# Kernel optimization log

Measured on AMD Instinct MI355X. Metric: run time of the kernel, lower is better.

The kernel has to match this reference:

```python
import jax, jax.numpy as jnp
import numpy as np

D_MODEL = 768
NUM_HEADS = 12
DIM_QKV = D_MODEL // NUM_HEADS  # 64
NEG_INF = -1000000000.0


def setup_inputs() -> dict:
    key = jax.random.key(0)
    ks = jax.random.split(key, 12)
    B, S = 2, 2048
    def lin(kw, kb):
        # torch nn.Linear default init: U(-1/sqrt(fan_in), 1/sqrt(fan_in))
        bound = 1.0 / np.sqrt(D_MODEL)
        W = jax.random.uniform(kw, (D_MODEL, D_MODEL), jnp.float32, -bound, bound)
        b = jax.random.uniform(kb, (D_MODEL,), jnp.float32, -bound, bound)
        return W, b
    Wq, bq = lin(ks[0], ks[1])
    Wk, bk = lin(ks[2], ks[3])
    Wv, bv = lin(ks[4], ks[5])
    Wo, bo = lin(ks[6], ks[7])
    Q = jax.random.normal(ks[8], (B, S, D_MODEL), jnp.float32)
    K = jax.random.normal(ks[9], (B, S, D_MODEL), jnp.float32)
    V = jax.random.normal(ks[10], (B, S, D_MODEL), jnp.float32)
    mask = jnp.tril(jnp.ones((S, S), dtype=bool))[None, None]  # [1,1,S,S] causal
    return {"Q": Q, "K": K, "V": V, "mask": mask,
            "Wq": Wq, "bq": bq, "Wk": Wk, "bk": bk,
            "Wv": Wv, "bv": bv, "Wo": Wo, "bo": bo}


def _split_heads(x):
    B, S, _ = x.shape
    return x.reshape(B, S, NUM_HEADS, DIM_QKV).transpose(0, 2, 1, 3)  # [B,H,S,d]


def reference(Q, K, V, mask, Wq, bq, Wk, bk, Wv, bv, Wo, bo):
    # torch Linear: y = x @ W.T + b
    q = _split_heads(Q @ Wq.T + bq)
    k = _split_heads(K @ Wk.T + bk)
    v = _split_heads(V @ Wv.T + bv)
    scale = jnp.sqrt(jnp.float32(DIM_QKV))
    scores = jnp.einsum('bhqd,bhkd->bhqk', q, k) / scale  # [B,H,S,S]
    scores = jnp.where(mask, scores, NEG_INF)
    probs = jax.nn.softmax(scores, axis=-1)  # dropout p=0 -> identity
    attn = jnp.einsum('bhqk,bhkd->bhqd', probs, v)
    B, H, S, d = attn.shape
    out = attn.transpose(0, 2, 1, 3).reshape(B, S, H * d) @ Wo.T + bo
    return out, scores
```

## Files before the change

### kernel.cpp

```cpp
#include <hip/hip_runtime.h>
#include <hip/hip_bf16.h>

typedef __attribute__((ext_vector_type(8))) short short8;
typedef __attribute__((ext_vector_type(4))) short short4v;
typedef __attribute__((ext_vector_type(4))) float f32x4;

#define S_LEN 2048
#define DM 768
#define NH 12
#define HD 64
#define NB 2
#define MROWS (NB*S_LEN)
#define NEGINF (-1.0e9f)
#define XEL 3145728
#define WEL 589824

__device__ __forceinline__ unsigned short f2bf(float x) {
    __hip_bfloat16 h = __float2bfloat16(x);
    return *reinterpret_cast<unsigned short*>(&h);
}

__device__ __forceinline__ void gl_lds16(const unsigned short* g, unsigned short* l) {
    __builtin_amdgcn_global_load_lds(
        (const __attribute__((address_space(1))) unsigned int*)g,
        (__attribute__((address_space(3))) unsigned int*)l, 16, 0, 0);
}

__global__ __launch_bounds__(256) void cvt_w_kernel(
    const float* w0, const float* w1, const float* w2, const float* w3,
    unsigned short* dst)
{
    int which = blockIdx.y;
    const float* src = (which == 0) ? w0 : (which == 1) ? w1 : (which == 2) ? w2 : w3;
    size_t idx = (size_t)blockIdx.x * 256 + threadIdx.x;
    const float* s = src + idx * 8;
    f32x4 v0 = *(const f32x4*)s;
    f32x4 v1 = *(const f32x4*)(s + 4);
    short8 o;
    o[0] = (short)f2bf(v0[0]); o[1] = (short)f2bf(v0[1]);
    o[2] = (short)f2bf(v0[2]); o[3] = (short)f2bf(v0[3]);
    o[4] = (short)f2bf(v1[0]); o[5] = (short)f2bf(v1[1]);
    o[6] = (short)f2bf(v1[2]); o[7] = (short)f2bf(v1[3]);
    *(short8*)&dst[(size_t)which * WEL + idx * 8] = o;
}

__global__ __launch_bounds__(256) void gemm_qkv_kernel(
    const float* Xq, const float* Xk, const float* Xv, const unsigned short* Wall,
    const float* b0, const float* b1, const float* b2, unsigned short* qh)
{
    int by = blockIdx.y;
    const float* A = (by == 0) ? Xq : (by == 1) ? Xk : Xv;
    const unsigned short* W = Wall + (size_t)by * WEL;
    const float* bias = (by == 0) ? b0 : (by == 1) ? b1 : b2;
    int bx = blockIdx.x;
    int im = (bx & 7) + 8 * (bx / 48);
    int jn = (bx >> 3) % 6;
    int i0 = im * 128, j0 = jn * 128;

    __shared__ unsigned short As[128 * 64];
    __shared__ unsigned short Ws[128 * 64];

    int t = threadIdx.x;
    int w = t >> 6, lane = t & 63, g = lane >> 4, fr = lane & 15;
    int wm = w >> 1, wn = w & 1;

    f32x4 acc[4][4];
    for (int i = 0; i < 4; ++i)
        for (int j = 0; j < 4; ++j)
            acc[i][j] = (f32x4){0.f, 0.f, 0.f, 0.f};

    int boff = t * 16;
    int arow = t >> 3;
    int acol = (t & 7) * 8;

    for (int k0 = 0; k0 < DM; k0 += 64) {
        __syncthreads();
        for (int r = 0; r < 4; ++r) {
            int b = r * 4096 + boff;
            int row = b >> 7, colb = b & 127;
            gl_lds16(&W[(size_t)(j0 + row) * DM + k0 + (colb >> 1)],
                     (unsigned short*)((char*)Ws + b));
        }
        for (int rr = 0; rr < 4; ++rr) {
            int row = rr * 32 + arow;
            const float* src = &A[(size_t)(i0 + row) * DM + k0 + acol];
            f32x4 v0 = *(const f32x4*)src;
            f32x4 v1 = *(const f32x4*)(src + 4);
            short8 o;
            o[0] = (short)f2bf(v0[0]); o[1] = (short)f2bf(v0[1]);
            o[2] = (short)f2bf(v0[2]); o[3] = (short)f2bf(v0[3]);
            o[4] = (short)f2bf(v1[0]); o[5] = (short)f2bf(v1[1]);
            o[6] = (short)f2bf(v1[2]); o[7] = (short)f2bf(v1[3]);
            *(short8*)&As[row * 64 + acol] = o;
        }
        __syncthreads();
        for (int kk = 0; kk < 2; ++kk) {
            short8 af[4], wf[4];
            for (int it = 0; it < 4; ++it)
                af[it] = *(const short8*)&As[(wm * 64 + it * 16 + fr) * 64 + kk * 32 + g * 8];
            for (int jt = 0; jt < 4; ++jt)
                wf[jt] = *(const short8*)&Ws[(wn * 64 + jt * 16 + fr) * 64 + kk * 32 + g * 8];
            for (int it = 0; it < 4; ++it)
                for (int jt = 0; jt < 4; ++jt)
                    acc[it][jt] = __builtin_amdgcn_mfma_f32_16x16x32_bf16(af[it], wf[jt], acc[it][jt], 0, 0, 0);
        }
    }

    float scl = (by == 0) ? 0.125f : 1.0f;
    if (by < 2) {
        unsigned short* outp = qh + (size_t)by * XEL;
        for (int jt = 0; jt < 4; ++jt) {
            int j = j0 + wn * 64 + jt * 16 + fr;
            float bv = bias[j];
            int h = j >> 6, dq = j & 63;
            for (int it = 0; it < 4; ++it)
                for (int r = 0; r < 4; ++r) {
                    int i = i0 + wm * 64 + it * 16 + g * 4 + r;
                    int bb = i >> 11, s = i & 2047;
                    outp[((size_t)((bb * NH + h) * S_LEN) + s) * HD + dq] = f2bf((acc[it][jt][r] + bv) * scl);
                }
        }
    } else {
        unsigned short* vtp = qh + (size_t)2 * XEL;
        for (int jt = 0; jt < 4; ++jt) {
            int j = j0 + wn * 64 + jt * 16 + fr;
            float bv = bias[j];
            int h = j >> 6, dq = j & 63;
            for (int it = 0; it < 4; ++it) {
                int ibase = i0 + wm * 64 + it * 16 + g * 4;
                int bb = ibase >> 11, s = ibase & 2047;
                short4v o;
                for (int r = 0; r < 4; ++r) o[r] = (short)f2bf(acc[it][jt][r] + bv);
                *(short4v*)&vtp[((size_t)(bb * NH + h) * HD + dq) * S_LEN + s] = o;
            }
        }
    }
}

__global__ __launch_bounds__(256) void gemm_o_kernel(
    const unsigned short* A, const unsigned short* W, const float* bias, float* f_out)
{
    int bx = blockIdx.x;
    int im = (bx & 7) + 8 * (bx / 96);
    int jn = (bx >> 3) % 12;
    int i0 = im * 64, j0 = jn * 64;

    __shared__ unsigned short As[64 * 64];
    __shared__ unsigned short Ws[64 * 64];

    int t = threadIdx.x;
    int w = t >> 6, lane = t & 63, g = lane >> 4, fr = lane & 15;
    int wm = w >> 1, wn = w & 1;

    f32x4 acc[2][2];
    for (int i = 0; i < 2; ++i)
        for (int j = 0; j < 2; ++j)
            acc[i][j] = (f32x4){0.f, 0.f, 0.f, 0.f};

    int boff = t * 16;

    for (int k0 = 0; k0 < DM; k0 += 64) {
        __syncthreads();
        for (int r = 0; r < 2; ++r) {
            int b = r * 4096 + boff;
            int row = b >> 7, colb = b & 127;
            gl_lds16(&A[(size_t)(i0 + row) * DM + k0 + (colb >> 1)],
                     (unsigned short*)((char*)As + b));
            gl_lds16(&W[(size_t)(j0 + row) * DM + k0 + (colb >> 1)],
                     (unsigned short*)((char*)Ws + b));
        }
        __syncthreads();
        for (int kk = 0; kk < 2; ++kk) {
            short8 af[2], wf[2];
            for (int it = 0; it < 2; ++it)
                af[it] = *(const short8*)&As[(wm * 32 + it * 16 + fr) * 64 + kk * 32 + g * 8];
            for (int jt = 0; jt < 2; ++jt)
                wf[jt] = *(const short8*)&Ws[(wn * 32 + jt * 16 + fr) * 64 + kk * 32 + g * 8];
            for (int it = 0; it < 2; ++it)
                for (int jt = 0; jt < 2; ++jt)
                    acc[it][jt] = __builtin_amdgcn_mfma_f32_16x16x32_bf16(af[it], wf[jt], acc[it][jt], 0, 0, 0);
        }
    }

    for (int jt = 0; jt < 2; ++jt) {
        int j = j0 + wn * 32 + jt * 16 + fr;
        float bv = bias[j];
        for (int it = 0; it < 2; ++it)
            for (int r = 0; r < 4; ++r) {
                int i = i0 + wm * 32 + it * 16 + g * 4 + r;
                f_out[(size_t)i * DM + j] = acc[it][jt][r] + bv;
            }
    }
}

__global__ __launch_bounds__(256) void attn_kernel(
    const unsigned short* q, const unsigned short* k, const unsigned short* vt,
    float* scores, unsigned short* attn)
{
    __shared__ unsigned short KV[2][8192];
    __shared__ float P[4][16][68];
    int t = threadIdx.x;
    int w = t >> 6, lane = t & 63, g = lane >> 4, fr = lane & 15;
    float (*Pw)[68] = P[w];

    int bid = blockIdx.x;
    int bh = (bid & 7) * 3 + (bid >> 3) % 3;
    int s = bid / 24;
    int myspan = (w < 2) ? s : 63 - s;
    int qbase = myspan * 32 + (w & 1) * 16;
    int myNt = ((myspan * 32 + 31) >> 6) + 1;
    int ntmax = (((63 - s) * 32 + 31) >> 6) + 1;
    int b = bh / NH, h = bh % NH;

    const unsigned short* qp = q + (size_t)bh * S_LEN * HD;
    const unsigned short* kp = k + (size_t)bh * S_LEN * HD;
    const unsigned short* vp = vt + (size_t)bh * HD * S_LEN;
    float* sp = scores + (size_t)bh * S_LEN * S_LEN;

    int srow2 = t >> 3;
    int scb = (t & 7) * 16;
    int swzu = (fr & 7) * 8;

    short8 qf0 = *(const short8*)&qp[(size_t)(qbase + fr) * HD + g * 8];
    short8 qf1 = *(const short8*)&qp[(size_t)(qbase + fr) * HD + 32 + g * 8];

    f32x4 acc[4];
    for (int jt = 0; jt < 4; ++jt) acc[jt] = (f32x4){0.f, 0.f, 0.f, 0.f};
    float m_run = -1e30f, l_run = 0.f;

    for (int rd = 0; rd < 2; ++rd) {
        int row = rd * 32 + srow2;
        int sc = (scb ^ ((row & 7) << 4)) >> 1;
        gl_lds16(&kp[(size_t)row * HD + sc], &KV[0][(size_t)t * 8 + rd * 2048]);
        gl_lds16(&vp[(size_t)row * S_LEN + sc], &KV[0][4096 + (size_t)t * 8 + rd * 2048]);
    }
    __builtin_amdgcn_sched_barrier(0);
    asm volatile("s_waitcnt vmcnt(0)" ::: "memory");
    __builtin_amdgcn_sched_barrier(0);
    __builtin_amdgcn_s_barrier();
    __builtin_amdgcn_sched_barrier(0);

    int buf = 0;
    for (int kt = 0; kt < ntmax; ++kt) {
        if (kt + 1 < ntmax) {
            int kb2 = (kt + 1) * 64;
            for (int rd = 0; rd < 2; ++rd) {
                int row = rd * 32 + srow2;
                int sc = (scb ^ ((row & 7) << 4)) >> 1;
                gl_lds16(&kp[(size_t)(kb2 + row) * HD + sc], &KV[buf ^ 1][(size_t)t * 8 + rd * 2048]);
                gl_lds16(&vp[(size_t)row * S_LEN + kb2 + sc], &KV[buf ^ 1][4096 + (size_t)t * 8 + rd * 2048]);
            }
        }
        __builtin_amdgcn_sched_barrier(0);
        if (kt < myNt) {
            const unsigned short* Kb = KV[buf];
            const unsigned short* Vb = KV[buf] + 4096;
            int kb = kt * 64;
            bool diag = (kt == myNt - 1);

            short8 kf[4][2];
            for (int ktt = 0; ktt < 4; ++ktt) {
                int base = (ktt * 16 + fr) * 64;
                kf[ktt][0] = *(const short8*)&Kb[base + ((g * 8) ^ swzu)];
                kf[ktt][1] = *(const short8*)&Kb[base + ((32 + g * 8) ^ swzu)];
            }
            __builtin_amdgcn_s_setprio(1);
            f32x4 s4v[4];
            for (int ktt = 0; ktt < 4; ++ktt) {
                f32x4 s4 = (f32x4){0.f, 0.f, 0.f, 0.f};
                s4 = __builtin_amdgcn_mfma_f32_16x16x32_bf16(qf0, kf[ktt][0], s4, 0, 0, 0);
                s4 = __builtin_amdgcn_mfma_f32_16x16x32_bf16(qf1, kf[ktt][1], s4, 0, 0, 0);
                s4v[ktt] = s4;
            }
            __builtin_amdgcn_s_setprio(0);
            if (diag) {
                for (int ktt = 0; ktt < 4; ++ktt) {
                    int kg = kb + ktt * 16 + fr;
                    for (int r = 0; r < 4; ++r) {
                        int qg = qbase + g * 4 + r;
                        float val = (kg <= qg) ? s4v[ktt][r] : NEGINF;
                        Pw[g * 4 + r][ktt * 16 + fr] = val;
                    }
                }
            } else {
                for (int ktt = 0; ktt < 4; ++ktt)
                    for (int r = 0; r < 4; ++r)
                        Pw[g * 4 + r][ktt * 16 + fr] = s4v[ktt][r];
            }
            for (int pass = 0; pass < 4; ++pass) {
                int rr = pass * 4 + g;
                int cc = fr * 4;
                f32x4 vv = *(const f32x4*)&Pw[rr][cc];
                __builtin_nontemporal_store(vv, (f32x4*)&sp[(size_t)(qbase + rr) * S_LEN + kb + cc]);
            }
            f32x4 pA = *(const f32x4*)&Pw[fr][g * 8];
            f32x4 pB = *(const f32x4*)&Pw[fr][g * 8 + 4];
            f32x4 pC = *(const f32x4*)&Pw[fr][32 + g * 8];
            f32x4 pD = *(const f32x4*)&Pw[fr][32 + g * 8 + 4];
            float pv[16];
            pv[0]=pA[0]; pv[1]=pA[1]; pv[2]=pA[2]; pv[3]=pA[3];
            pv[4]=pB[0]; pv[5]=pB[1]; pv[6]=pB[2]; pv[7]=pB[3];
            pv[8]=pC[0]; pv[9]=pC[1]; pv[10]=pC[2]; pv[11]=pC[3];
            pv[12]=pD[0]; pv[13]=pD[1]; pv[14]=pD[2]; pv[15]=pD[3];
            float tmax = pv[0];
            for (int e = 1; e < 16; ++e) tmax = fmaxf(tmax, pv[e]);
            tmax = fmaxf(tmax, __shfl_xor(tmax, 16, 64));
            tmax = fmaxf(tmax, __shfl_xor(tmax, 32, 64));
            float m_new = fmaxf(m_run, tmax);
            float corr = __expf(m_run - m_new);
            float lsum = 0.f;
            for (int e = 0; e < 16; ++e) { pv[e] = __expf(pv[e] - m_new); lsum += pv[e]; }
            lsum += __shfl_xor(lsum, 16, 64);
            lsum += __shfl_xor(lsum, 32, 64);
            l_run = l_run * corr + lsum;
            m_run = m_new;
            short8 pa0, pa1;
            for (int e = 0; e < 8; ++e) { pa0[e] = (short)f2bf(pv[e]); pa1[e] = (short)f2bf(pv[8 + e]); }
            float fc[4];
            for (int r = 0; r < 4; ++r) fc[r] = __shfl(corr, g * 4 + r, 64);
            for (int jt = 0; jt < 4; ++jt)
                for (int r = 0; r < 4; ++r) acc[jt][r] *= fc[r];
            short8 vf[4][2];
            for (int jt = 0; jt < 4; ++jt) {
                int base = (jt * 16 + fr) * 64;
                vf[jt][0] = *(const short8*)&Vb[base + ((g * 8) ^ swzu)];
                vf[jt][1] = *(const short8*)&Vb[base + ((32 + g * 8) ^ swzu)];
            }
            __builtin_amdgcn_s_setprio(1);
            for (int jt = 0; jt < 4; ++jt) {
                acc[jt] = __builtin_amdgcn_mfma_f32_16x16x32_bf16(pa0, vf[jt][0], acc[jt], 0, 0, 0);
                acc[jt] = __builtin_amdgcn_mfma_f32_16x16x32_bf16(pa1, vf[jt][1], acc[jt], 0, 0, 0);
            }
            __builtin_amdgcn_s_setprio(0);
        }
        if (kt + 1 < ntmax) {
            __builtin_amdgcn_sched_barrier(0);
            if (kt < myNt) asm volatile("s_waitcnt vmcnt(4)" ::: "memory");
            else           asm volatile("s_waitcnt vmcnt(0)" ::: "memory");
            __builtin_amdgcn_sched_barrier(0);
            __builtin_amdgcn_s_barrier();
            __builtin_amdgcn_sched_barrier(0);
        }
        buf ^= 1;
    }
    float linv[4];
    for (int r = 0; r < 4; ++r) linv[r] = 1.0f / __shfl(l_run, g * 4 + r, 64);
    for (int jt = 0; jt < 4; ++jt) {
        int col = h * HD + jt * 16 + fr;
        for (int r = 0; r < 4; ++r) {
            int i = b * S_LEN + qbase + g * 4 + r;
            attn[(size_t)i * DM + col] = f2bf(acc[jt][r] * linv[r]);
        }
    }
    f32x4 nv = (f32x4){NEGINF, NEGINF, NEGINF, NEGINF};
    int fill0 = myNt * 64;
    for (int rr = 0; rr < 16; ++rr) {
        float* rowp = &sp[(size_t)(qbase + rr) * S_LEN];
        for (int c = fill0 + lane * 4; c < S_LEN; c += 256)
            __builtin_nontemporal_store(nv, (f32x4*)(rowp + c));
    }
}

extern "C" void kernel_launch(void* const* d_in, const int* in_sizes, int n_in,
                              void* d_out, int out_size, void* d_ws, size_t ws_size,
                              hipStream_t stream) {
    const float* Q  = (const float*)d_in[0];
    const float* K  = (const float*)d_in[1];
    const float* V  = (const float*)d_in[2];
    const float* Wq = (const float*)d_in[4];
    const float* bq = (const float*)d_in[5];
    const float* Wk = (const float*)d_in[6];
    const float* bk = (const float*)d_in[7];
    const float* Wv = (const float*)d_in[8];
    const float* bv = (const float*)d_in[9];
    const float* Wo = (const float*)d_in[10];
    const float* bo = (const float*)d_in[11];

    float* out = (float*)d_out;
    float* scores = out + (size_t)MROWS * DM;

    unsigned short* ws   = (unsigned short*)d_ws;
    unsigned short* Wbf  = ws;
    unsigned short* qh   = Wbf + (size_t)4 * WEL;
    unsigned short* attn = qh + (size_t)3 * XEL;

    cvt_w_kernel<<<dim3(288, 4), 256, 0, stream>>>(Wq, Wk, Wv, Wo, Wbf);
    gemm_qkv_kernel<<<dim3(192, 3), 256, 0, stream>>>(Q, K, V, Wbf, bq, bk, bv, qh);
    attn_kernel<<<dim3(768), 256, 0, stream>>>(qh, qh + (size_t)XEL, qh + (size_t)2 * XEL,
                                               scores, attn);
    gemm_o_kernel<<<dim3(768), 256, 0, stream>>>(attn, Wbf + (size_t)3 * WEL, bo, out);
}
```

Measured before the change: 158.2 us.

## Compute transposed S^T tiles to drop LDS score staging in attention

Swaps the MFMA operand order so each lane holds a query row's scores across key columns. Score stores, row max/sum and P-to-bf16 packing then work directly from registers, which removes the per-warp LDS P buffer and its round trip. The V^T layout written by the projection kernel is permuted within 32-element groups so the P operand matches the new register layout, and the attention output is written as vectorized short4 stores. The risk is correctness of the permutation mapping and less-coalesced score stores, since each lane now writes 16-byte pieces of different rows.

```diff
diff --git a/kernel.cpp b/kernel.cpp
--- a/kernel.cpp
+++ b/kernel.cpp
@@ -129,9 +129,10 @@
             for (int it = 0; it < 4; ++it) {
                 int ibase = i0 + wm * 64 + it * 16 + g * 4;
                 int bb = ibase >> 11, s = ibase & 2047;
+                int ps = (s & ~31) | ((((s >> 2) & 3) << 3) | (((s >> 4) & 1) << 2));
                 short4v o;
                 for (int r = 0; r < 4; ++r) o[r] = (short)f2bf(acc[it][jt][r] + bv);
-                *(short4v*)&vtp[((size_t)(bb * NH + h) * HD + dq) * S_LEN + s] = o;
+                *(short4v*)&vtp[((size_t)(bb * NH + h) * HD + dq) * S_LEN + ps] = o;
             }
         }
     }
@@ -198,10 +199,8 @@
     float* scores, unsigned short* attn)
 {
     __shared__ unsigned short KV[2][8192];
-    __shared__ float P[4][16][68];
     int t = threadIdx.x;
     int w = t >> 6, lane = t & 63, g = lane >> 4, fr = lane & 15;
-    float (*Pw)[68] = P[w];
 
     int bid = blockIdx.x;
     int bh = (bid & 7) * 3 + (bid >> 3) % 3;
@@ -211,6 +210,7 @@
     int myNt = ((myspan * 32 + 31) >> 6) + 1;
     int ntmax = (((63 - s) * 32 + 31) >> 6) + 1;
     int b = bh / NH, h = bh % NH;
+    int qg = qbase + fr;
 
     const unsigned short* qp = q + (size_t)bh * S_LEN * HD;
     const unsigned short* kp = k + (size_t)bh * S_LEN * HD;
@@ -221,8 +221,8 @@
     int scb = (t & 7) * 16;
     int swzu = (fr & 7) * 8;
 
-    short8 qf0 = *(const short8*)&qp[(size_t)(qbase + fr) * HD + g * 8];
-    short8 qf1 = *(const short8*)&qp[(size_t)(qbase + fr) * HD + 32 + g * 8];
+    short8 qf0 = *(const short8*)&qp[(size_t)qg * HD + g * 8];
+    short8 qf1 = *(const short8*)&qp[(size_t)qg * HD + 32 + g * 8];
 
     f32x4 acc[4];
     for (int jt = 0; jt < 4; ++jt) acc[jt] = (f32x4){0.f, 0.f, 0.f, 0.f};
@@ -268,58 +268,46 @@
             f32x4 s4v[4];
             for (int ktt = 0; ktt < 4; ++ktt) {
                 f32x4 s4 = (f32x4){0.f, 0.f, 0.f, 0.f};
-                s4 = __builtin_amdgcn_mfma_f32_16x16x32_bf16(qf0, kf[ktt][0], s4, 0, 0, 0);
-                s4 = __builtin_amdgcn_mfma_f32_16x16x32_bf16(qf1, kf[ktt][1], s4, 0, 0, 0);
+                s4 = __builtin_amdgcn_mfma_f32_16x16x32_bf16(kf[ktt][0], qf0, s4, 0, 0, 0);
+                s4 = __builtin_amdgcn_mfma_f32_16x16x32_bf16(kf[ktt][1], qf1, s4, 0, 0, 0);
                 s4v[ktt] = s4;
             }
             __builtin_amdgcn_s_setprio(0);
             if (diag) {
-                for (int ktt = 0; ktt < 4; ++ktt) {
-                    int kg = kb + ktt * 16 + fr;
+                for (int ktt = 0; ktt < 4; ++ktt)
                     for (int r = 0; r < 4; ++r) {
-                        int qg = qbase + g * 4 + r;
-                        float val = (kg <= qg) ? s4v[ktt][r] : NEGINF;
-                        Pw[g * 4 + r][ktt * 16 + fr] = val;
+                        int kg = kb + ktt * 16 + g * 4 + r;
+                        if (kg > qg) s4v[ktt][r] = NEGINF;
                     }
-                }
-            } else {
-                for (int ktt = 0; ktt < 4; ++ktt)
-                    for (int r = 0; r < 4; ++r)
-                        Pw[g * 4 + r][ktt * 16 + fr] = s4v[ktt][r];
-            }
-            for (int pass = 0; pass < 4; ++pass) {
-                int rr = pass * 4 + g;
-                int cc = fr * 4;
-                f32x4 vv = *(const f32x4*)&Pw[rr][cc];
-                __builtin_nontemporal_store(vv, (f32x4*)&sp[(size_t)(qbase + rr) * S_LEN + kb + cc]);
-            }
-            f32x4 pA = *(const f32x4*)&Pw[fr][g * 8];
-            f32x4 pB = *(const f32x4*)&Pw[fr][g * 8 + 4];
-            f32x4 pC = *(const f32x4*)&Pw[fr][32 + g * 8];
-            f32x4 pD = *(const f32x4*)&Pw[fr][32 + g * 8 + 4];
-            float pv[16];
-            pv[0]=pA[0]; pv[1]=pA[1]; pv[2]=pA[2]; pv[3]=pA[3];
-            pv[4]=pB[0]; pv[5]=pB[1]; pv[6]=pB[2]; pv[7]=pB[3];
-            pv[8]=pC[0]; pv[9]=pC[1]; pv[10]=pC[2]; pv[11]=pC[3];
-            pv[12]=pD[0]; pv[13]=pD[1]; pv[14]=pD[2]; pv[15]=pD[3];
-            float tmax = pv[0];
-            for (int e = 1; e < 16; ++e) tmax = fmaxf(tmax, pv[e]);
+            }
+            for (int ktt = 0; ktt < 4; ++ktt)
+                __builtin_nontemporal_store(s4v[ktt],
+                    (f32x4*)&sp[(size_t)qg * S_LEN + kb + ktt * 16 + g * 4]);
+            float tmax = s4v[0][0];
+            for (int ktt = 0; ktt < 4; ++ktt)
+                for (int r = 0; r < 4; ++r) tmax = fmaxf(tmax, s4v[ktt][r]);
             tmax = fmaxf(tmax, __shfl_xor(tmax, 16, 64));
             tmax = fmaxf(tmax, __shfl_xor(tmax, 32, 64));
             float m_new = fmaxf(m_run, tmax);
             float corr = __expf(m_run - m_new);
             float lsum = 0.f;
-            for (int e = 0; e < 16; ++e) { pv[e] = __expf(pv[e] - m_new); lsum += pv[e]; }
+            for (int ktt = 0; ktt < 4; ++ktt)
+                for (int r = 0; r < 4; ++r) {
+                    float e = __expf(s4v[ktt][r] - m_new);
+                    s4v[ktt][r] = e;
+                    lsum += e;
+                }
             lsum += __shfl_xor(lsum, 16, 64);
             lsum += __shfl_xor(lsum, 32, 64);
             l_run = l_run * corr + lsum;
             m_run = m_new;
-            short8 pa0, pa1;
-            for (int e = 0; e < 8; ++e) { pa0[e] = (short)f2bf(pv[e]); pa1[e] = (short)f2bf(pv[8 + e]); }
-            float fc[4];
-            for (int r = 0; r < 4; ++r) fc[r] = __shfl(corr, g * 4 + r, 64);
             for (int jt = 0; jt < 4; ++jt)
-                for (int r = 0; r < 4; ++r) acc[jt][r] *= fc[r];
+                for (int r = 0; r < 4; ++r) acc[jt][r] *= corr;
+            short8 pb0, pb1;
+            for (int e = 0; e < 8; ++e) {
+                pb0[e] = (short)f2bf(s4v[e >> 2][e & 3]);
+                pb1[e] = (short)f2bf(s4v[2 + (e >> 2)][e & 3]);
+            }
             short8 vf[4][2];
             for (int jt = 0; jt < 4; ++jt) {
                 int base = (jt * 16 + fr) * 64;
@@ -328,8 +316,8 @@
             }
             __builtin_amdgcn_s_setprio(1);
             for (int jt = 0; jt < 4; ++jt) {
-                acc[jt] = __builtin_amdgcn_mfma_f32_16x16x32_bf16(pa0, vf[jt][0], acc[jt], 0, 0, 0);
-                acc[jt] = __builtin_amdgcn_mfma_f32_16x16x32_bf16(pa1, vf[jt][1], acc[jt], 0, 0, 0);
+                acc[jt] = __builtin_amdgcn_mfma_f32_16x16x32_bf16(vf[jt][0], pb0, acc[jt], 0, 0, 0);
+                acc[jt] = __builtin_amdgcn_mfma_f32_16x16x32_bf16(vf[jt][1], pb1, acc[jt], 0, 0, 0);
             }
             __builtin_amdgcn_s_setprio(0);
         }
@@ -343,14 +331,12 @@
         }
         buf ^= 1;
     }
-    float linv[4];
-    for (int r = 0; r < 4; ++r) linv[r] = 1.0f / __shfl(l_run, g * 4 + r, 64);
+    float linv = 1.0f / l_run;
+    size_t arow = (size_t)(b * S_LEN + qg) * DM + h * HD;
     for (int jt = 0; jt < 4; ++jt) {
-        int col = h * HD + jt * 16 + fr;
-        for (int r = 0; r < 4; ++r) {
-            int i = b * S_LEN + qbase + g * 4 + r;
-            attn[(size_t)i * DM + col] = f2bf(acc[jt][r] * linv[r]);
-        }
+        short4v o;
+        for (int r = 0; r < 4; ++r) o[r] = (short)f2bf(acc[jt][r] * linv);
+        *(short4v*)&attn[arow + jt * 16 + g * 4] = o;
     }
     f32x4 nv = (f32x4){NEGINF, NEGINF, NEGINF, NEGINF};
     int fill0 = myNt * 64;
```

After: 183.9 us. +16.3%, slower.
